# Optimization experiments

Measured on AMD Instinct MI355X. Metric: run time of the kernel, lower is better.

## Reference

```python
import jax, jax.numpy as jnp
import numpy as np

N_NODES = 50000
N_EDGES = 800000


def setup_inputs() -> dict:
    key = jax.random.key(0)
    ks = jax.random.split(key, 8)
    return {
        "x": jax.random.normal(ks[0], (N_NODES, 256), dtype=jnp.float32),
        "adj_vals": jax.random.uniform(ks[1], (N_EDGES,), dtype=jnp.float32),
        "rows": jax.random.randint(ks[2], (N_EDGES,), 0, N_NODES, dtype=jnp.int32),
        "cols": jax.random.randint(ks[3], (N_EDGES,), 0, N_NODES, dtype=jnp.int32),
        "W1": jax.random.normal(ks[4], (256, 256), dtype=jnp.float32) * (1.0 / np.sqrt(256)),
        "b1": jnp.zeros((256,), dtype=jnp.float32),
        "W2": jax.random.normal(ks[5], (256, 256), dtype=jnp.float32) * (1.0 / np.sqrt(256)),
        "b2": jnp.zeros((256,), dtype=jnp.float32),
        "W3": jax.random.normal(ks[6], (256, 128), dtype=jnp.float32) * (1.0 / np.sqrt(256)),
        "b3": jnp.zeros((128,), dtype=jnp.float32),
    }


def reference(x, adj_vals, rows, cols, W1, b1, W2, b2, W3, b3):
    n = x.shape[0]

    def spmm(h):
        # sparse adjacency matmul: out[r] += val * h[c] over all edges (r, c)
        return jax.ops.segment_sum(adj_vals[:, None] * h[cols], rows, num_segments=n)

    # GCNLayer: adj @ (x @ W) + b ; ReLU between layers (dropout p=0 => identity)
    h = jax.nn.relu(spmm(x @ W1) + b1)
    h = jax.nn.relu(spmm(h @ W2) + b2)
    return spmm(h @ W3) + b3
```

## Files before the change

### kernel.cpp

```cpp
#include <hip/hip_runtime.h>
#include <hip/hip_bf16.h>


#define N_NODES 50000
#define N_EDGES 800000
#define KDIM 256
#define NB_SCAN 49
#define COUNTS_PAD (NB_SCAN * 1024)

typedef __attribute__((ext_vector_type(8))) short short8;
typedef __attribute__((ext_vector_type(4))) float f32x4;

__device__ __forceinline__ ushort f2bf(float f) {
    union { float f; unsigned u; } x; x.f = f;
    unsigned r = x.u + 0x7fffu + ((x.u >> 16) & 1u);
    return (ushort)(r >> 16);
}
__device__ __forceinline__ float bf2f(ushort u) {
    union { unsigned u; float f; } x; x.u = ((unsigned)u) << 16;
    return x.f;
}

__global__ __launch_bounds__(256) void transpose_w_kernel(const float* __restrict__ W,
                                                          ushort* __restrict__ Wt, int Ndim) {
    int id = blockIdx.x * blockDim.x + threadIdx.x;
    if (id < Ndim * KDIM) {
        int nrow = id >> 8;
        int k    = id & 255;
        Wt[nrow * KDIM + k] = f2bf(W[k * Ndim + nrow]);
    }
}


__global__ void hist_kernel(const int* __restrict__ rows, int* __restrict__ counts, int ne) {
    int e = blockIdx.x * blockDim.x + threadIdx.x;
    if (e < ne) atomicAdd(&counts[rows[e]], 1);
}

__global__ __launch_bounds__(256) void scan_sums(const int* __restrict__ counts,
                                                 int* __restrict__ bsum) {
    __shared__ int ws[4];
    int b = blockIdx.x, t = threadIdx.x, lane = t & 63, wv = t >> 6;
    int4 v = *(const int4*)&counts[b * 1024 + t * 4];
    int s = v.x + v.y + v.z + v.w;
    #pragma unroll
    for (int off = 32; off >= 1; off >>= 1) s += __shfl_down(s, off, 64);
    if (lane == 0) ws[wv] = s;
    __syncthreads();
    if (t == 0) bsum[b] = ws[0] + ws[1] + ws[2] + ws[3];
}

__global__ __launch_bounds__(64) void scan_block(const int* __restrict__ bsum,
                                                 int* __restrict__ boff,
                                                 int* __restrict__ rp, int nb, int n) {
    int t = threadIdx.x;
    int v = (t < nb) ? bsum[t] : 0;
    int incl = v;
    #pragma unroll
    for (int off = 1; off < 64; off <<= 1) {
        int u = __shfl_up(incl, off, 64);
        if (t >= off) incl += u;
    }
    if (t < nb) boff[t] = incl - v;
    if (t == 63) rp[n] = incl;
}

__global__ __launch_bounds__(256) void scan_apply(int* __restrict__ counts,
                                                  const int* __restrict__ boff,
                                                  int* __restrict__ rp, int n) {
    __shared__ int ws[4];
    int b = blockIdx.x, t = threadIdx.x, lane = t & 63, wv = t >> 6;
    int i = b * 1024 + t * 4;
    int4 v = *(const int4*)&counts[i];
    int s0 = v.x, s01 = s0 + v.y, s012 = s01 + v.z, tsum = s012 + v.w;
    int incl = tsum;
    #pragma unroll
    for (int off = 1; off < 64; off <<= 1) {
        int u = __shfl_up(incl, off, 64);
        if (lane >= off) incl += u;
    }
    if (lane == 63) ws[wv] = incl;
    __syncthreads();
    int woff = 0;
    #pragma unroll
    for (int j = 0; j < 3; j++) woff += (j < wv) ? ws[j] : 0;
    int base = boff[b] + woff + incl - tsum;
    if (i < n)     rp[i]     = base;
    if (i + 1 < n) rp[i + 1] = base + s0;
    if (i + 2 < n) rp[i + 2] = base + s01;
    if (i + 3 < n) rp[i + 3] = base + s012;
    *(int4*)&counts[i] = make_int4(0, 0, 0, 0);
}

__global__ void scatter_kernel(const int* __restrict__ rows, const int* __restrict__ cols,
                               const float* __restrict__ vals, const int* __restrict__ rp,
                               int* __restrict__ counts, int2* __restrict__ cv, int ne) {
    int e = blockIdx.x * blockDim.x + threadIdx.x;
    if (e < ne) {
        int r = rows[e];
        int pos = rp[r] + atomicAdd(&counts[r], 1);
        cv[pos] = make_int2(cols[e], __float_as_int(vals[e]));
    }
}


#define LDK 40

template <bool AFP32>
__global__ __launch_bounds__(256) void gemm_bf16_kernel(
        const void* __restrict__ Ain, const ushort* __restrict__ Wt,
        ushort* __restrict__ C, int M, int N) {
    __shared__ ushort As[128 * LDK];
    __shared__ ushort Ws[128 * LDK];

    int t = threadIdx.x;
    int lane = t & 63;
    int w = t >> 6;
    int row0 = blockIdx.x * 128, col0 = blockIdx.y * 128;
    int wm = (w & 1) * 64, wn = (w >> 1) * 64;
    int q = lane >> 4, mi = lane & 15;

    int r0 = t >> 2, kc = (t & 3) * 8;

    f32x4 acc[4][4];
    #pragma unroll
    for (int i = 0; i < 4; i++)
        #pragma unroll
        for (int j = 0; j < 4; j++) acc[i][j] = (f32x4)0.f;

    for (int k0 = 0; k0 < KDIM; k0 += 32) {
        int ga0 = row0 + r0;       if (ga0 >= M) ga0 = M - 1;
        int ga1 = row0 + r0 + 64;  if (ga1 >= M) ga1 = M - 1;
        short8 a0, a1;
        if (AFP32) {
            const float* Af = (const float*)Ain;
            float4 f0 = *(const float4*)&Af[ga0 * KDIM + k0 + kc];
            float4 f1 = *(const float4*)&Af[ga0 * KDIM + k0 + kc + 4];
            float4 f2 = *(const float4*)&Af[ga1 * KDIM + k0 + kc];
            float4 f3 = *(const float4*)&Af[ga1 * KDIM + k0 + kc + 4];
            a0[0] = (short)f2bf(f0.x); a0[1] = (short)f2bf(f0.y);
            a0[2] = (short)f2bf(f0.z); a0[3] = (short)f2bf(f0.w);
            a0[4] = (short)f2bf(f1.x); a0[5] = (short)f2bf(f1.y);
            a0[6] = (short)f2bf(f1.z); a0[7] = (short)f2bf(f1.w);
            a1[0] = (short)f2bf(f2.x); a1[1] = (short)f2bf(f2.y);
            a1[2] = (short)f2bf(f2.z); a1[3] = (short)f2bf(f2.w);
            a1[4] = (short)f2bf(f3.x); a1[5] = (short)f2bf(f3.y);
            a1[6] = (short)f2bf(f3.z); a1[7] = (short)f2bf(f3.w);
        } else {
            const ushort* Ab = (const ushort*)Ain;
            a0 = *(const short8*)&Ab[ga0 * KDIM + k0 + kc];
            a1 = *(const short8*)&Ab[ga1 * KDIM + k0 + kc];
        }
        short8 b0 = *(const short8*)&Wt[(col0 + r0) * KDIM + k0 + kc];
        short8 b1 = *(const short8*)&Wt[(col0 + r0 + 64) * KDIM + k0 + kc];
        __syncthreads();
        *(short8*)&As[r0 * LDK + kc]        = a0;
        *(short8*)&As[(r0 + 64) * LDK + kc] = a1;
        *(short8*)&Ws[r0 * LDK + kc]        = b0;
        *(short8*)&Ws[(r0 + 64) * LDK + kc] = b1;
        __syncthreads();

        short8 af[4], bf[4];
        #pragma unroll
        for (int mt = 0; mt < 4; mt++)
            af[mt] = *(const short8*)&As[(wm + mt * 16 + mi) * LDK + q * 8];
        #pragma unroll
        for (int nt = 0; nt < 4; nt++)
            bf[nt] = *(const short8*)&Ws[(wn + nt * 16 + mi) * LDK + q * 8];
        #pragma unroll
        for (int mt = 0; mt < 4; mt++)
            #pragma unroll
            for (int nt = 0; nt < 4; nt++)
                acc[mt][nt] = __builtin_amdgcn_mfma_f32_16x16x32_bf16(
                    af[mt], bf[nt], acc[mt][nt], 0, 0, 0);
    }

    #pragma unroll
    for (int mt = 0; mt < 4; mt++) {
        #pragma unroll
        for (int r = 0; r < 4; r++) {
            int grow = row0 + wm + mt * 16 + q * 4 + r;
            if (grow < M) {
                #pragma unroll
                for (int nt = 0; nt < 4; nt++) {
                    int gcol = col0 + wn + nt * 16 + mi;
                    C[grow * N + gcol] = f2bf(acc[mt][nt][r]);
                }
            }
        }
    }
}


template <int F, bool RELU, bool OUT_BF16>
__global__ __launch_bounds__(256) void spmm_kernel(
        const ushort* __restrict__ H, const int* __restrict__ rp,
        const int2* __restrict__ cv, const float* __restrict__ bias,
        void* __restrict__ out, int nrows) {
    constexpr int FL = F / 8;
    constexpr int EP = 64 / FL;
    int wave = threadIdx.x >> 6, lane = threadIdx.x & 63;
    int r = blockIdx.x * 4 + wave;
    if (r >= nrows) return;
    int fl = lane % FL, ep = lane / FL;
    const ushort* Hl = H + fl * 8;

    float acc[8];
    #pragma unroll
    for (int j = 0; j < 8; j++) acc[j] = 0.f;

    int start = rp[r], end = rp[r + 1];
    for (int base = start; base < end; base += 2 * EP) {
        int e0 = base + ep, e1 = base + EP + ep;
        bool p0 = e0 < end, p1 = e1 < end;
        int2 m0 = p0 ? cv[e0] : make_int2(0, 0);
        int2 m1 = p1 ? cv[e1] : make_int2(0, 0);
        float v0 = __int_as_float(m0.y);
        float v1 = __int_as_float(m1.y);
        short8 h0 = *(const short8*)&Hl[(size_t)m0.x * F];
        short8 h1 = *(const short8*)&Hl[(size_t)m1.x * F];
        #pragma unroll
        for (int j = 0; j < 8; j++)
            acc[j] += v0 * bf2f((ushort)h0[j]) + v1 * bf2f((ushort)h1[j]);
    }

    #pragma unroll
    for (int off = FL; off < 64; off <<= 1)
        #pragma unroll
        for (int j = 0; j < 8; j++) acc[j] += __shfl_down(acc[j], off, 64);

    if (ep == 0) {
        #pragma unroll
        for (int j = 0; j < 8; j++) {
            float o = acc[j] + bias[fl * 8 + j];
            if (RELU) o = fmaxf(o, 0.f);
            acc[j] = o;
        }
        if (OUT_BF16) {
            short8 ob;
            #pragma unroll
            for (int j = 0; j < 8; j++) ob[j] = (short)f2bf(acc[j]);
            *(short8*)((ushort*)out + (size_t)r * F + fl * 8) = ob;
        } else {
            float* of = (float*)out + (size_t)r * F + fl * 8;
            *(float4*)&of[0] = make_float4(acc[0], acc[1], acc[2], acc[3]);
            *(float4*)&of[4] = make_float4(acc[4], acc[5], acc[6], acc[7]);
        }
    }
}


extern "C" void kernel_launch(void* const* d_in, const int* in_sizes, int n_in,
                              void* d_out, int out_size, void* d_ws, size_t ws_size,
                              hipStream_t stream) {
    const float* x    = (const float*)d_in[0];
    const float* av   = (const float*)d_in[1];
    const int*   rows = (const int*)d_in[2];
    const int*   cols = (const int*)d_in[3];
    const float* W1   = (const float*)d_in[4];
    const float* b1   = (const float*)d_in[5];
    const float* W2   = (const float*)d_in[6];
    const float* b2   = (const float*)d_in[7];
    const float* W3   = (const float*)d_in[8];
    const float* b3   = (const float*)d_in[9];
    float* out = (float*)d_out;

    const int N = N_NODES, E = N_EDGES;

    char* p = (char*)d_ws;
    auto carve = [&](size_t bytes) {
        void* q = (void*)p;
        p += (bytes + 255) & ~(size_t)255;
        return q;
    };
    ushort* bufG = (ushort*)carve((size_t)N * 256 * 2);
    ushort* bufH = (ushort*)carve((size_t)N * 256 * 2);
    ushort* Wt1  = (ushort*)carve((size_t)256 * 256 * 2);
    ushort* Wt2  = (ushort*)carve((size_t)256 * 256 * 2);
    ushort* Wt3  = (ushort*)carve((size_t)128 * 256 * 2);
    int*    rp     = (int*)carve((size_t)(N + 1) * 4);
    int*    counts = (int*)carve((size_t)COUNTS_PAD * 4);
    int*    bsum   = (int*)carve((size_t)NB_SCAN * 4);
    int*    boff   = (int*)carve((size_t)NB_SCAN * 4);
    int2*   cv     = (int2*)carve((size_t)E * 8);

    hipMemsetAsync(counts, 0, (size_t)COUNTS_PAD * 4, stream);
    transpose_w_kernel<<<(256 * 256 + 255) / 256, 256, 0, stream>>>(W1, Wt1, 256);
    transpose_w_kernel<<<(256 * 256 + 255) / 256, 256, 0, stream>>>(W2, Wt2, 256);
    transpose_w_kernel<<<(128 * 256 + 255) / 256, 256, 0, stream>>>(W3, Wt3, 128);
    hist_kernel<<<(E + 255) / 256, 256, 0, stream>>>(rows, counts, E);
    scan_sums<<<NB_SCAN, 256, 0, stream>>>(counts, bsum);
    scan_block<<<1, 64, 0, stream>>>(bsum, boff, rp, NB_SCAN, N);
    scan_apply<<<NB_SCAN, 256, 0, stream>>>(counts, boff, rp, N);
    scatter_kernel<<<(E + 255) / 256, 256, 0, stream>>>(rows, cols, av, rp, counts, cv, E);

    dim3 g2((N + 127) / 128, 2);
    dim3 g1((N + 127) / 128, 1);
    int spmm_blocks = (N + 3) / 4;

    gemm_bf16_kernel<true><<<g2, 256, 0, stream>>>(x, Wt1, bufG, N, 256);
    spmm_kernel<256, true, true><<<spmm_blocks, 256, 0, stream>>>(bufG, rp, cv, b1, bufH, N);
    gemm_bf16_kernel<false><<<g2, 256, 0, stream>>>(bufH, Wt2, bufG, N, 256);
    spmm_kernel<256, true, true><<<spmm_blocks, 256, 0, stream>>>(bufG, rp, cv, b2, bufH, N);
    gemm_bf16_kernel<false><<<g1, 256, 0, stream>>>(bufH, Wt3, bufG, N, 128);
    spmm_kernel<128, false, false><<<spmm_blocks, 256, 0, stream>>>(bufG, rp, cv, b3, out, N);
}
```

Baseline: 404.4 us.

## Fuse histogram into first GEMM, spread row counters, unroll SpMM gather by four

Merges the three weight transposes into one launch, and folds the edge histogram into the first GEMM launch as extra blocks so the two can overlap. Row counters are replicated eight ways by edge index, which is meant to cut atomic contention in the histogram and scatter, at the cost of a longer scan (400k entries, multi-wave block scan). The SpMM loop now loads four consecutive edges per lane instead of two strided ones, raising memory-level parallelism. It can read up to 16 entries past the end of cv, which is padded for this, and the layout still groups edges by row so results are unchanged apart from summation order.

```diff
diff --git a/kernel.cpp b/kernel.cpp
--- a/kernel.cpp
+++ b/kernel.cpp
@@ -5,8 +5,10 @@
 #define N_NODES 50000
 #define N_EDGES 800000
 #define KDIM 256
-#define NB_SCAN 49
-#define COUNTS_PAD (NB_SCAN * 1024)
+#define REP 8
+#define NC (N_NODES * REP)
+#define NB2 ((NC + 1023) / 1024)
+#define NC_PAD (NB2 * 1024)
 
 typedef __attribute__((ext_vector_type(8))) short short8;
 typedef __attribute__((ext_vector_type(4))) float f32x4;
@@ -21,85 +23,20 @@
     return x.f;
 }
 
-__global__ __launch_bounds__(256) void transpose_w_kernel(const float* __restrict__ W,
-                                                          ushort* __restrict__ Wt, int Ndim) {
+__global__ __launch_bounds__(256) void transpose_all_kernel(
+        const float* __restrict__ W1, const float* __restrict__ W2,
+        const float* __restrict__ W3, ushort* __restrict__ Wt1,
+        ushort* __restrict__ Wt2, ushort* __restrict__ Wt3) {
     int id = blockIdx.x * blockDim.x + threadIdx.x;
-    if (id < Ndim * KDIM) {
-        int nrow = id >> 8;
-        int k    = id & 255;
-        Wt[nrow * KDIM + k] = f2bf(W[k * Ndim + nrow]);
-    }
-}
-
-
-__global__ void hist_kernel(const int* __restrict__ rows, int* __restrict__ counts, int ne) {
-    int e = blockIdx.x * blockDim.x + threadIdx.x;
-    if (e < ne) atomicAdd(&counts[rows[e]], 1);
-}
-
-__global__ __launch_bounds__(256) void scan_sums(const int* __restrict__ counts,
-                                                 int* __restrict__ bsum) {
-    __shared__ int ws[4];
-    int b = blockIdx.x, t = threadIdx.x, lane = t & 63, wv = t >> 6;
-    int4 v = *(const int4*)&counts[b * 1024 + t * 4];
-    int s = v.x + v.y + v.z + v.w;
-    #pragma unroll
-    for (int off = 32; off >= 1; off >>= 1) s += __shfl_down(s, off, 64);
-    if (lane == 0) ws[wv] = s;
-    __syncthreads();
-    if (t == 0) bsum[b] = ws[0] + ws[1] + ws[2] + ws[3];
-}
-
-__global__ __launch_bounds__(64) void scan_block(const int* __restrict__ bsum,
-                                                 int* __restrict__ boff,
-                                                 int* __restrict__ rp, int nb, int n) {
-    int t = threadIdx.x;
-    int v = (t < nb) ? bsum[t] : 0;
-    int incl = v;
-    #pragma unroll
-    for (int off = 1; off < 64; off <<= 1) {
-        int u = __shfl_up(incl, off, 64);
-        if (t >= off) incl += u;
-    }
-    if (t < nb) boff[t] = incl - v;
-    if (t == 63) rp[n] = incl;
-}
-
-__global__ __launch_bounds__(256) void scan_apply(int* __restrict__ counts,
-                                                  const int* __restrict__ boff,
-                                                  int* __restrict__ rp, int n) {
-    __shared__ int ws[4];
-    int b = blockIdx.x, t = threadIdx.x, lane = t & 63, wv = t >> 6;
-    int i = b * 1024 + t * 4;
-    int4 v = *(const int4*)&counts[i];
-    int s0 = v.x, s01 = s0 + v.y, s012 = s01 + v.z, tsum = s012 + v.w;
-    int incl = tsum;
-    #pragma unroll
-    for (int off = 1; off < 64; off <<= 1) {
-        int u = __shfl_up(incl, off, 64);
-        if (lane >= off) incl += u;
-    }
-    if (lane == 63) ws[wv] = incl;
-    __syncthreads();
-    int woff = 0;
-    #pragma unroll
-    for (int j = 0; j < 3; j++) woff += (j < wv) ? ws[j] : 0;
-    int base = boff[b] + woff + incl - tsum;
-    if (i < n)     rp[i]     = base;
-    if (i + 1 < n) rp[i + 1] = base + s0;
-    if (i + 2 < n) rp[i + 2] = base + s01;
-    if (i + 3 < n) rp[i + 3] = base + s012;
-    *(int4*)&counts[i] = make_int4(0, 0, 0, 0);
-}
-
-__global__ void scatter_kernel(const int* __restrict__ rows, const int* __restrict__ cols,
-                               const float* __restrict__ vals, const int* __restrict__ rp,
-                               int* __restrict__ counts, int2* __restrict__ cv, int ne) {
-    int e = blockIdx.x * blockDim.x + threadIdx.x;
-    if (e < ne) {
-        int r = rows[e];
-        int pos = rp[r] + atomicAdd(&counts[r], 1);
-        cv[pos] = make_int2(cols[e], __float_as_int(vals[e]));
+    if (id < 65536) {
+        int n = id >> 8, k = id & 255;
+        Wt1[n * 256 + k] = f2bf(W1[k * 256 + n]);
+    } else if (id < 131072) {
+        int i = id - 65536, n = i >> 8, k = i & 255;
+        Wt2[n * 256 + k] = f2bf(W2[k * 256 + n]);
+    } else if (id < 163840) {
+        int i = id - 131072, n = i >> 8, k = i & 255;
+        Wt3[n * 256 + k] = f2bf(W3[k * 128 + n]);
     }
 }
 
@@ -107,19 +44,18 @@
 #define LDK 40
 
 template <bool AFP32>
-__global__ __launch_bounds__(256) void gemm_bf16_kernel(
+__device__ __forceinline__ void gemm_body(
         const void* __restrict__ Ain, const ushort* __restrict__ Wt,
-        ushort* __restrict__ C, int M, int N) {
+        ushort* __restrict__ C, int M, int N, int bx, int by) {
     __shared__ ushort As[128 * LDK];
     __shared__ ushort Ws[128 * LDK];
 
     int t = threadIdx.x;
     int lane = t & 63;
     int w = t >> 6;
-    int row0 = blockIdx.x * 128, col0 = blockIdx.y * 128;
+    int row0 = bx * 128, col0 = by * 128;
     int wm = (w & 1) * 64, wn = (w >> 1) * 64;
     int q = lane >> 4, mi = lane & 15;
-
     int r0 = t >> 2, kc = (t & 3) * 8;
 
     f32x4 acc[4][4];
@@ -191,14 +127,113 @@
     }
 }
 
+#define GB1 782
+
+__global__ __launch_bounds__(256) void gemm1_hist_kernel(
+        const float* __restrict__ x, const ushort* __restrict__ Wt1,
+        ushort* __restrict__ C, const int* __restrict__ rows,
+        int* __restrict__ counts) {
+    int b = blockIdx.x;
+    if (b < GB1) {
+        gemm_body<true>(x, Wt1, C, N_NODES, 256, b % 391, b / 391);
+    } else {
+        int e = (b - GB1) * 256 + threadIdx.x;
+        if (e < N_EDGES) {
+            int r = rows[e];
+            atomicAdd(&counts[(r << 3) | (e & 7)], 1);
+        }
+    }
+}
+
+template <bool AFP32>
+__global__ __launch_bounds__(256) void gemm_bf16_kernel(
+        const void* __restrict__ Ain, const ushort* __restrict__ Wt,
+        ushort* __restrict__ C, int M, int N) {
+    gemm_body<AFP32>(Ain, Wt, C, M, N, blockIdx.x, blockIdx.y);
+}
+
+
+__global__ __launch_bounds__(256) void scan_sums(const int* __restrict__ counts,
+                                                 int* __restrict__ bsum) {
+    __shared__ int ws[4];
+    int b = blockIdx.x, t = threadIdx.x, lane = t & 63, wv = t >> 6;
+    int4 v = *(const int4*)&counts[b * 1024 + t * 4];
+    int s = v.x + v.y + v.z + v.w;
+    #pragma unroll
+    for (int off = 32; off >= 1; off >>= 1) s += __shfl_down(s, off, 64);
+    if (lane == 0) ws[wv] = s;
+    __syncthreads();
+    if (t == 0) bsum[b] = ws[0] + ws[1] + ws[2] + ws[3];
+}
+
+__global__ __launch_bounds__(512) void scan_block(const int* __restrict__ bsum,
+                                                  int* __restrict__ boff,
+                                                  int* __restrict__ rp8, int nb) {
+    __shared__ int ws[8];
+    int t = threadIdx.x, lane = t & 63, wv = t >> 6;
+    int v = (t < nb) ? bsum[t] : 0;
+    int incl = v;
+    #pragma unroll
+    for (int off = 1; off < 64; off <<= 1) {
+        int u = __shfl_up(incl, off, 64);
+        if (lane >= off) incl += u;
+    }
+    if (lane == 63) ws[wv] = incl;
+    __syncthreads();
+    int wo = 0;
+    #pragma unroll
+    for (int j = 0; j < 7; j++) wo += (j < wv) ? ws[j] : 0;
+    if (t < nb) boff[t] = wo + incl - v;
+    if (t == 511) rp8[NC] = wo + incl;
+}
+
+__global__ __launch_bounds__(256) void scan_apply(int* __restrict__ counts,
+                                                  const int* __restrict__ boff,
+                                                  int* __restrict__ rp8) {
+    __shared__ int ws[4];
+    int b = blockIdx.x, t = threadIdx.x, lane = t & 63, wv = t >> 6;
+    int i = b * 1024 + t * 4;
+    int4 v = *(const int4*)&counts[i];
+    int s0 = v.x, s01 = s0 + v.y, s012 = s01 + v.z, tsum = s012 + v.w;
+    int incl = tsum;
+    #pragma unroll
+    for (int off = 1; off < 64; off <<= 1) {
+        int u = __shfl_up(incl, off, 64);
+        if (lane >= off) incl += u;
+    }
+    if (lane == 63) ws[wv] = incl;
+    __syncthreads();
+    int woff = 0;
+    #pragma unroll
+    for (int j = 0; j < 3; j++) woff += (j < wv) ? ws[j] : 0;
+    int base = boff[b] + woff + incl - tsum;
+    if (i < NC)     rp8[i]     = base;
+    if (i + 1 < NC) rp8[i + 1] = base + s0;
+    if (i + 2 < NC) rp8[i + 2] = base + s01;
+    if (i + 3 < NC) rp8[i + 3] = base + s012;
+    *(int4*)&counts[i] = make_int4(0, 0, 0, 0);
+}
+
+__global__ void scatter_kernel(const int* __restrict__ rows, const int* __restrict__ cols,
+                               const float* __restrict__ vals, const int* __restrict__ rp8,
+                               int* __restrict__ counts, int2* __restrict__ cv) {
+    int e = blockIdx.x * blockDim.x + threadIdx.x;
+    if (e < N_EDGES) {
+        int idx = (rows[e] << 3) | (e & 7);
+        int pos = rp8[idx] + atomicAdd(&counts[idx], 1);
+        cv[pos] = make_int2(cols[e], __float_as_int(vals[e]));
+    }
+}
+
 
 template <int F, bool RELU, bool OUT_BF16>
 __global__ __launch_bounds__(256) void spmm_kernel(
-        const ushort* __restrict__ H, const int* __restrict__ rp,
+        const ushort* __restrict__ H, const int* __restrict__ rp8,
         const int2* __restrict__ cv, const float* __restrict__ bias,
         void* __restrict__ out, int nrows) {
     constexpr int FL = F / 8;
     constexpr int EP = 64 / FL;
+    constexpr int STEP = EP * 4;
     int wave = threadIdx.x >> 6, lane = threadIdx.x & 63;
     int r = blockIdx.x * 4 + wave;
     if (r >= nrows) return;
@@ -209,19 +244,26 @@
     #pragma unroll
     for (int j = 0; j < 8; j++) acc[j] = 0.f;
 
-    int start = rp[r], end = rp[r + 1];
-    for (int base = start; base < end; base += 2 * EP) {
-        int e0 = base + ep, e1 = base + EP + ep;
-        bool p0 = e0 < end, p1 = e1 < end;
-        int2 m0 = p0 ? cv[e0] : make_int2(0, 0);
-        int2 m1 = p1 ? cv[e1] : make_int2(0, 0);
-        float v0 = __int_as_float(m0.y);
-        float v1 = __int_as_float(m1.y);
-        short8 h0 = *(const short8*)&Hl[(size_t)m0.x * F];
-        short8 h1 = *(const short8*)&Hl[(size_t)m1.x * F];
+    int start = rp8[r * REP], end = rp8[r * REP + REP];
+    for (int base = start; base < end; base += STEP) {
+        int e0 = base + ep * 4;
+        int2 m0 = cv[e0], m1 = cv[e0 + 1], m2 = cv[e0 + 2], m3 = cv[e0 + 3];
+        int   c0 = (e0     < end) ? m0.x : 0;
+        int   c1 = (e0 + 1 < end) ? m1.x : 0;
+        int   c2 = (e0 + 2 < end) ? m2.x : 0;
+        int   c3 = (e0 + 3 < end) ? m3.x : 0;
+        float v0 = (e0     < end) ? __int_as_float(m0.y) : 0.f;
+        float v1 = (e0 + 1 < end) ? __int_as_float(m1.y) : 0.f;
+        float v2 = (e0 + 2 < end) ? __int_as_float(m2.y) : 0.f;
+        float v3 = (e0 + 3 < end) ? __int_as_float(m3.y) : 0.f;
+        short8 h0 = *(const short8*)&Hl[(size_t)c0 * F];
+        short8 h1 = *(const short8*)&Hl[(size_t)c1 * F];
+        short8 h2 = *(const short8*)&Hl[(size_t)c2 * F];
+        short8 h3 = *(const short8*)&Hl[(size_t)c3 * F];
         #pragma unroll
         for (int j = 0; j < 8; j++)
-            acc[j] += v0 * bf2f((ushort)h0[j]) + v1 * bf2f((ushort)h1[j]);
+            acc[j] += v0 * bf2f((ushort)h0[j]) + v1 * bf2f((ushort)h1[j])
+                    + v2 * bf2f((ushort)h2[j]) + v3 * bf2f((ushort)h3[j]);
     }
 
     #pragma unroll
@@ -278,30 +320,26 @@
     ushort* Wt1  = (ushort*)carve((size_t)256 * 256 * 2);
     ushort* Wt2  = (ushort*)carve((size_t)256 * 256 * 2);
     ushort* Wt3  = (ushort*)carve((size_t)128 * 256 * 2);
-    int*    rp     = (int*)carve((size_t)(N + 1) * 4);
-    int*    counts = (int*)carve((size_t)COUNTS_PAD * 4);
-    int*    bsum   = (int*)carve((size_t)NB_SCAN * 4);
-    int*    boff   = (int*)carve((size_t)NB_SCAN * 4);
-    int2*   cv     = (int2*)carve((size_t)E * 8);
-
-    hipMemsetAsync(counts, 0, (size_t)COUNTS_PAD * 4, stream);
-    transpose_w_kernel<<<(256 * 256 + 255) / 256, 256, 0, stream>>>(W1, Wt1, 256);
-    transpose_w_kernel<<<(256 * 256 + 255) / 256, 256, 0, stream>>>(W2, Wt2, 256);
-    transpose_w_kernel<<<(128 * 256 + 255) / 256, 256, 0, stream>>>(W3, Wt3, 128);
-    hist_kernel<<<(E + 255) / 256, 256, 0, stream>>>(rows, counts, E);
-    scan_sums<<<NB_SCAN, 256, 0, stream>>>(counts, bsum);
-    scan_block<<<1, 64, 0, stream>>>(bsum, boff, rp, NB_SCAN, N);
-    scan_apply<<<NB_SCAN, 256, 0, stream>>>(counts, boff, rp, N);
-    scatter_kernel<<<(E + 255) / 256, 256, 0, stream>>>(rows, cols, av, rp, counts, cv, E);
-
-    dim3 g2((N + 127) / 128, 2);
-    dim3 g1((N + 127) / 128, 1);
+    int*    rp8    = (int*)carve((size_t)(NC + 1) * 4);
+    int*    counts = (int*)carve((size_t)NC_PAD * 4);
+    int*    bsum   = (int*)carve((size_t)NB2 * 4);
+    int*    boff   = (int*)carve((size_t)NB2 * 4);
+    int2*   cv     = (int2*)carve((size_t)(E + 16) * 8);
+
+    hipMemsetAsync(counts, 0, (size_t)NC_PAD * 4, stream);
+    transpose_all_kernel<<<(163840 + 255) / 256, 256, 0, stream>>>(W1, W2, W3, Wt1, Wt2, Wt3);
+
+    gemm1_hist_kernel<<<GB1 + (E + 255) / 256, 256, 0, stream>>>(x, Wt1, bufG, rows, counts);
+
+    scan_sums<<<NB2, 256, 0, stream>>>(counts, bsum);
+    scan_block<<<1, 512, 0, stream>>>(bsum, boff, rp8, NB2);
+    scan_apply<<<NB2, 256, 0, stream>>>(counts, boff, rp8);
+    scatter_kernel<<<(E + 255) / 256, 256, 0, stream>>>(rows, cols, av, rp8, counts, cv);
+
     int spmm_blocks = (N + 3) / 4;
-
-    gemm_bf16_kernel<true><<<g2, 256, 0, stream>>>(x, Wt1, bufG, N, 256);
-    spmm_kernel<256, true, true><<<spmm_blocks, 256, 0, stream>>>(bufG, rp, cv, b1, bufH, N);
-    gemm_bf16_kernel<false><<<g2, 256, 0, stream>>>(bufH, Wt2, bufG, N, 256);
-    spmm_kernel<256, true, true><<<spmm_blocks, 256, 0, stream>>>(bufG, rp, cv, b2, bufH, N);
-    gemm_bf16_kernel<false><<<g1, 256, 0, stream>>>(bufH, Wt3, bufG, N, 128);
-    spmm_kernel<128, false, false><<<spmm_blocks, 256, 0, stream>>>(bufG, rp, cv, b3, out, N);
-}
+    spmm_kernel<256, true, true><<<spmm_blocks, 256, 0, stream>>>(bufG, rp8, cv, b1, bufH, N);
+    gemm_bf16_kernel<false><<<dim3(391, 2), 256, 0, stream>>>(bufH, Wt2, bufG, N, 256);
+    spmm_kernel<256, true, true><<<spmm_blocks, 256, 0, stream>>>(bufG, rp8, cv, b2, bufH, N);
+    gemm_bf16_kernel<false><<<dim3(391, 1), 256, 0, stream>>>(bufH, Wt3, bufG, N, 128);
+    spmm_kernel<128, false, false><<<spmm_blocks, 256, 0, stream>>>(bufG, rp8, cv, b3, out, N);
+}
```

Measured after the change: 373.2 us. 1.08x faster.
